# Optimization experiments

Measured on AMD Instinct MI355X. Metric: run time of the kernel, lower is better.

## Reference

```python
import jax, jax.numpy as jnp
import numpy as np

N_EMBD = 1024
N_HEAD = 16
HEAD_DIM = N_EMBD // N_HEAD


def setup_inputs() -> dict:
    key = jax.random.key(0)
    ks = jax.random.split(key, 5)
    B, T = 4, 2048
    s = 0.02
    return {
        "x": jax.random.normal(ks[0], (B, T, N_EMBD), dtype=jnp.float32),
        "w_qkv": jax.random.normal(ks[1], (N_EMBD, 3 * N_EMBD), dtype=jnp.float32) * s,
        "b_qkv": jnp.zeros((3 * N_EMBD,), dtype=jnp.float32),
        "w_out": jax.random.normal(ks[2], (N_EMBD, N_EMBD), dtype=jnp.float32) * s,
        "b_out": jnp.zeros((N_EMBD,), dtype=jnp.float32),
    }


def reference(x, w_qkv, b_qkv, w_out, b_out):
    # Eval-mode forward (dropout disabled), matching the torch module's math.
    B, T, C = x.shape
    qkv = x @ w_qkv + b_qkv                      # [B,T,3C]
    q, k, v = jnp.split(qkv, 3, axis=-1)
    def heads(t):
        return t.reshape(B, T, N_HEAD, HEAD_DIM).transpose(0, 2, 1, 3)  # [B,H,T,D]
    q, k, v = heads(q), heads(k), heads(v)
    scores = jnp.einsum("bhtd,bhsd->bhts", q, k) / jnp.sqrt(jnp.float32(HEAD_DIM))
    causal = jnp.tril(jnp.ones((T, T), dtype=bool))
    scores = jnp.where(causal[None, None], scores, -jnp.inf)
    attn = jax.nn.softmax(scores, axis=-1)       # [B,H,T,T]
    y = jnp.einsum("bhts,bhsd->bhtd", attn, v)   # [B,H,T,D]
    y = y.transpose(0, 2, 1, 3).reshape(B, T, C)
    return y @ w_out + b_out
```

## Files before the change

kernel.cpp:

```cpp
#include <hip/hip_runtime.h>
#include <hip/hip_bf16.h>

#define TSEQ 2048
#define CEMB 1024

typedef __attribute__((ext_vector_type(8))) short bf16x8;
typedef __attribute__((ext_vector_type(4))) float f32x4;
typedef __attribute__((ext_vector_type(16))) float f32x16;
typedef __attribute__((ext_vector_type(4))) int i32x4;

__device__ __forceinline__ unsigned short f2bf(float f){
  return __builtin_bit_cast(unsigned short, __float2bfloat16(f));
}

__device__ __forceinline__ f32x4 MFMA16(bf16x8 a, bf16x8 b, f32x4 c){
  return __builtin_amdgcn_mfma_f32_16x16x32_bf16(a, b, c, 0, 0, 0);
}

#define GLDS(src, dst) __builtin_amdgcn_global_load_lds( \
      (const __attribute__((address_space(1))) void*)(src), \
      (__attribute__((address_space(3))) void*)(dst), 16, 0, 0)

template<int N> __device__ __forceinline__ void vmwait(){
  if constexpr (N == 0) asm volatile("s_waitcnt vmcnt(0)" ::: "memory");
  else if constexpr (N == 6) asm volatile("s_waitcnt vmcnt(6)" ::: "memory");
  else if constexpr (N == 7) asm volatile("s_waitcnt vmcnt(7)" ::: "memory");
  else asm volatile("s_waitcnt vmcnt(8)" ::: "memory");
}

__global__ void k_cvt_bf16(const float* __restrict__ in, unsigned short* __restrict__ out, int n4){
  int i = blockIdx.x * blockDim.x + threadIdx.x;
  if (i >= n4) return;
  const float4 v = reinterpret_cast<const float4*>(in)[i];
  ushort4 o;
  o.x = f2bf(v.x); o.y = f2bf(v.y); o.z = f2bf(v.z); o.w = f2bf(v.w);
  reinterpret_cast<ushort4*>(out)[i] = o;
}

__global__ void k_transpose_bf16(const float* __restrict__ w, unsigned short* __restrict__ wT, int K, int N){
  __shared__ unsigned short tile[32][33];
  const int n0 = blockIdx.x * 32, k0 = blockIdx.y * 32;
  const int tx = threadIdx.x & 31, ty = threadIdx.x >> 5;
  #pragma unroll
  for (int r = 0; r < 4; ++r){
    int k = ty * 4 + r;
    tile[k][tx] = f2bf(w[(size_t)(k0 + k) * N + n0 + tx]);
  }
  __syncthreads();
  #pragma unroll
  for (int r = 0; r < 4; ++r){
    int n = ty * 4 + r;
    wT[(size_t)(n0 + n) * K + k0 + tx] = tile[tx][n];
  }
}

__global__ __launch_bounds__(256) void k_vT(const unsigned short* __restrict__ qkv,
                                            unsigned short* __restrict__ vT){
  __shared__ __align__(16) unsigned short tile[64*64];
  const int tid = threadIdx.x;
  const int bh = blockIdx.x;
  const int t0 = blockIdx.y * 64;
  const int b = bh >> 4, h = bh & 15;
  const int lt = tid >> 3, seg = tid & 7;
  #pragma unroll
  for (int r = 0; r < 2; ++r){
    const int t = lt + 32*r;
    const i32x4 v = *(const i32x4*)&qkv[((size_t)(b*TSEQ + t0 + t))*3072 + 2048 + h*64 + seg*8];
    const int slot = seg ^ (t & 7) ^ (t >> 3);
    *(i32x4*)((char*)tile + t*128 + slot*16) = v;
  }
  __syncthreads();
  const int w = tid >> 6, lane = tid & 63;
  const int tseg = lane & 7;
  #pragma unroll
  for (int r = 0; r < 2; ++r){
    const int d = w*8 + (lane>>3) + 32*r;
    unsigned int wd[4];
    #pragma unroll
    for (int jp = 0; jp < 4; ++jp){
      unsigned int lo, hi;
      #pragma unroll
      for (int e = 0; e < 2; ++e){
        const int j = jp*2 + e;
        const int t = tseg*8 + j;
        const int byteoff = t*128 + ((2*d) ^ (((j ^ tseg) & 7) << 4));
        const unsigned int val = *(const unsigned short*)((const char*)tile + byteoff);
        if (e == 0) lo = val; else hi = val;
      }
      wd[jp] = lo | (hi << 16);
    }
    i32x4 o4; o4[0]=wd[0]; o4[1]=wd[1]; o4[2]=wd[2]; o4[3]=wd[3];
    *(i32x4*)&vT[((size_t)bh*64 + d)*2048 + t0 + tseg*8] = o4;
  }
}

template<bool OUT_BF16, int BN>
__global__ __launch_bounds__(512, 2) void k_gemm256(
    const unsigned short* __restrict__ A,
    const unsigned short* __restrict__ Bt,
    const float* __restrict__ bias,
    void* __restrict__ Cout, int M, int N, int K)
{
  constexpr int NW  = BN / 64;
  constexpr int NH0 = (NW + 1) / 2;
  constexpr int NL  = 4 + NW;
  constexpr int BNB = BN * 128;
  __shared__ __align__(16) char smem[65536 + 2 * BNB];

  const int tid = threadIdx.x;
  const int lane = tid & 63, w = tid >> 6;
  const int wm = w >> 2, wn = w & 3;
  const int l15 = lane & 15, l4 = lane >> 4;
  const int x7 = l15 & 7;

  unsigned lin = blockIdx.x;
  {
    const unsigned nwg = gridDim.x;
    const unsigned qq = nwg >> 3, rr = nwg & 7;
    const unsigned xcd = lin & 7, loc = lin >> 3;
    lin = (xcd < rr ? xcd * (qq + 1) : rr * (qq + 1) + (xcd - rr) * qq) + loc;
  }
  const unsigned ntn = (unsigned)N / BN;
  const int m0 = (int)(lin / ntn) << 8;
  const int n0 = (int)(lin % ntn) * BN;

  const int srow = lane >> 3;
  const int scx  = (lane & 7) ^ srow;
  const unsigned short* Ag = A  + (size_t)(m0 + w*8 + srow) * K + scx * 8;
  const unsigned short* Bg = Bt + (size_t)(n0 + w*8 + srow) * K + scx * 8;

  auto stageA = [&](int buf, int kt){
    const unsigned short* s = Ag + kt*64;
    char* d = smem + buf*32768 + (w << 10);
    #pragma unroll
    for (int i = 0; i < 4; ++i) GLDS(s + (size_t)(i*64)*K, d + i*8192);
  };
  auto stageB = [&](int buf, int kt){
    const unsigned short* s = Bg + kt*64;
    char* d = smem + 65536 + buf*BNB + (w << 10);
    #pragma unroll
    for (int i = 0; i < NW; ++i) GLDS(s + (size_t)(i*64)*K, d + i*8192);
  };

  const int arow = wm*128 + l15;
  const int brow = wn*(BN/4) + l15;
  auto rdA = [&](int buf, int m, int ks)->bf16x8 {
    return *(const bf16x8*)(smem + buf*32768 + (arow + m*16)*128 + (((ks*4 + l4) ^ x7) << 4));
  };
  auto rdB = [&](int buf, int n, int ks)->bf16x8 {
    return *(const bf16x8*)(smem + 65536 + buf*BNB + (brow + n*16)*128 + (((ks*4 + l4) ^ x7) << 4));
  };

  f32x4 acc[8][NW] = {};
  const int NIT = K >> 7;

  stageA(0, 0); stageB(0, 0);
  stageA(1, 1); stageB(1, 1);
  vmwait<NL>();
  __builtin_amdgcn_s_barrier();
  asm volatile("" ::: "memory");

  for (int it = 0; it < NIT; ++it){
    const bool more = (it + 1 < NIT);
    #pragma unroll
    for (int half = 0; half < 2; ++half){
      const int buf = half;
      bf16x8 bfr[NW][2], af1[4][2], af2[4][2];
      #pragma unroll
      for (int n = 0; n < NW; ++n){ bfr[n][0] = rdB(buf, n, 0); bfr[n][1] = rdB(buf, n, 1); }
      #pragma unroll
      for (int m = 0; m < 4; ++m){ af1[m][0] = rdA(buf, m, 0); af1[m][1] = rdA(buf, m, 1); }
      __builtin_amdgcn_s_setprio(1);
      #pragma unroll
      for (int m = 0; m < 4; ++m)
        #pragma unroll
        for (int n = 0; n < NH0; ++n)
          #pragma unroll
          for (int ks = 0; ks < 2; ++ks)
            acc[m][n] = MFMA16(af1[m][ks], bfr[n][ks], acc[m][n]);
      __builtin_amdgcn_s_setprio(0);
      #pragma unroll
      for (int m = 0; m < 4; ++m){ af2[m][0] = rdA(buf, m+4, 0); af2[m][1] = rdA(buf, m+4, 1); }
      __builtin_amdgcn_s_setprio(1);
      #pragma unroll
      for (int m = 0; m < 4; ++m)
        #pragma unroll
        for (int n = NH0; n < NW; ++n)
          #pragma unroll
          for (int ks = 0; ks < 2; ++ks)
            acc[m][n] = MFMA16(af1[m][ks], bfr[n][ks], acc[m][n]);
      __builtin_amdgcn_s_setprio(0);
      __builtin_amdgcn_s_setprio(1);
      #pragma unroll
      for (int m = 0; m < 4; ++m)
        #pragma unroll
        for (int n = NH0; n < NW; ++n)
          #pragma unroll
          for (int ks = 0; ks < 2; ++ks)
            acc[m+4][n] = MFMA16(af2[m][ks], bfr[n][ks], acc[m+4][n]);
      __builtin_amdgcn_s_setprio(0);
      asm volatile("s_waitcnt lgkmcnt(0)" ::: "memory");
      __builtin_amdgcn_s_barrier();
      asm volatile("" ::: "memory");
      if (more){ stageA(buf, 2*it + half + 2); stageB(buf, 2*it + half + 2); }
      __builtin_amdgcn_s_setprio(1);
      #pragma unroll
      for (int m = 0; m < 4; ++m)
        #pragma unroll
        for (int n = 0; n < NH0; ++n)
          #pragma unroll
          for (int ks = 0; ks < 2; ++ks)
            acc[m+4][n] = MFMA16(af2[m][ks], bfr[n][ks], acc[m+4][n]);
      __builtin_amdgcn_s_setprio(0);
      if (more) vmwait<NL>();
      else      vmwait<0>();
      __builtin_amdgcn_s_barrier();
      asm volatile("" ::: "memory");
    }
  }

  float bv[NW];
  #pragma unroll
  for (int n = 0; n < NW; ++n) bv[n] = bias[n0 + wn*(BN/4) + n*16 + l15];

  #pragma unroll
  for (int m = 0; m < 8; ++m){
    const int row = m0 + wm*128 + m*16 + l4*4;
    #pragma unroll
    for (int n = 0; n < NW; ++n){
      const int col = n0 + wn*(BN/4) + n*16 + l15;
      #pragma unroll
      for (int r = 0; r < 4; ++r){
        float v = acc[m][n][r] + bv[n];
        if (OUT_BF16)
          ((unsigned short*)Cout)[(size_t)(row + r) * N + col] = f2bf(v);
        else
          ((float*)Cout)[(size_t)(row + r) * N + col] = v;
      }
    }
  }
}

__global__ __launch_bounds__(512, 4) void k_attn(
    const unsigned short* __restrict__ qkv,
    const unsigned short* __restrict__ vT,
    unsigned short* __restrict__ y)
{
  __shared__ __align__(16) char Ksm[2][8192];
  __shared__ __align__(16) char Vsm[2][8192];
  __shared__ float Ls[8][32];

  const int tid = threadIdx.x, lane = tid & 63, w = tid >> 6;
  const int q31 = lane & 31, hi = lane >> 5;
  const int bh = blockIdx.x, p = blockIdx.y;
  const int g = w >> 2, wl = w & 3;
  const int myt = g ? (15 - p) : p;
  const int b = bh >> 4, h = bh & 15;
  const size_t rowB = (size_t)b * TSEQ;

  const int wq0 = myt*128 + 32*wl, qg = wq0 + q31;
  const int nkt_my = 2*myt + 2;
  const int nktB  = 2*(15 - p) + 2;

  const float sc = 0.18033688011112042f;

  bf16x8 qf[4];
  {
    const unsigned short* qp = qkv + (rowB + qg) * 3072 + h * 64;
    #pragma unroll
    for (int c4 = 0; c4 < 4; ++c4){
      bf16x8 v = *(const bf16x8*)(qp + c4*16 + hi*8);
      #pragma unroll
      for (int j = 0; j < 8; ++j){
        const unsigned int bits = ((unsigned int)(unsigned short)v[j]) << 16;
        v[j] = (short)f2bf(__builtin_bit_cast(float, bits) * sc);
      }
      qf[c4] = v;
    }
  }

  const int kr = lane >> 3, sl = lane & 7, cx = sl ^ kr;
  const unsigned short* kgbase = qkv + (rowB + w*8 + kr) * 3072 + 1024 + h*64 + cx*8;
  const unsigned short* vgbase = vT + ((size_t)bh*64 + w*8 + kr) * 2048 + cx*8;

  #define STAGE(ktile, buf)                                                          \
    do {                                                                             \
      GLDS(kgbase + (size_t)(ktile)*64*3072, &Ksm[buf][0] + w*1024);                 \
      GLDS(vgbase + (ktile)*64,              &Vsm[buf][0] + w*1024);                 \
    } while (0)

  f32x16 O[2] = {};
  float l = 0.f;

  STAGE(0, 0);
  __syncthreads();

  int cbuf = 0;
  for (int kt = 0; kt < nktB; ++kt){
    if (kt + 1 < nktB) STAGE(kt + 1, cbuf ^ 1);

    if (kt < nkt_my){
      const char* kb = Ksm[cbuf];
      const char* vb = Vsm[cbuf];
      const bool domask = (kt*64 + 63 > wq0);
      #pragma unroll
      for (int sub = 0; sub < 2; ++sub){
        f32x16 S = {};
        __builtin_amdgcn_s_setprio(1);
        #pragma unroll
        for (int c4 = 0; c4 < 4; ++c4){
          const bf16x8 kf = *(const bf16x8*)(kb + (sub*32 + q31)*128
                                + ((((c4<<1)|hi) ^ (q31 & 7)) << 4));
          S = __builtin_amdgcn_mfma_f32_32x32x16_bf16(kf, qf[c4], S, 0, 0, 0);
        }
        __builtin_amdgcn_s_setprio(0);
        if (domask){
          #pragma unroll
          for (int r = 0; r < 16; ++r){
            const int kg = kt*64 + sub*32 + (r&3) + 8*(r>>2) + 4*hi;
            if (kg > qg) S[r] = -1e30f;
          }
        }
        float ps = 0.f;
        #pragma unroll
        for (int r = 0; r < 16; ++r){
          S[r] = __builtin_amdgcn_exp2f(S[r]);
          ps += S[r];
        }
        l += ps;
        bf16x8 paf[2];
        #pragma unroll
        for (int kc = 0; kc < 2; ++kc){
          const int e = kc * 8;
          unsigned int a, bb, cc, dd;
          asm("v_cvt_pk_bf16_f32 %0, %1, %2" : "=v"(a)  : "v"(S[e+0]), "v"(S[e+1]));
          asm("v_cvt_pk_bf16_f32 %0, %1, %2" : "=v"(bb) : "v"(S[e+4]), "v"(S[e+5]));
          asm("v_cvt_pk_bf16_f32 %0, %1, %2" : "=v"(cc) : "v"(S[e+2]), "v"(S[e+3]));
          asm("v_cvt_pk_bf16_f32 %0, %1, %2" : "=v"(dd) : "v"(S[e+6]), "v"(S[e+7]));
          asm volatile("v_permlane32_swap_b32 %0, %1" : "+v"(a),  "+v"(bb));
          asm volatile("v_permlane32_swap_b32 %0, %1" : "+v"(cc), "+v"(dd));
          i32x4 pwv; pwv[0] = (int)a; pwv[1] = (int)cc; pwv[2] = (int)bb; pwv[3] = (int)dd;
          paf[kc] = __builtin_bit_cast(bf16x8, pwv);
        }
        __builtin_amdgcn_s_setprio(1);
        #pragma unroll
        for (int kc = 0; kc < 2; ++kc){
          #pragma unroll
          for (int dblk = 0; dblk < 2; ++dblk){
            const int dr = dblk*32 + q31;
            const bf16x8 vf = *(const bf16x8*)(vb + dr*128
                                  + ((((sub<<2)|(kc<<1)|hi) ^ (dr & 7)) << 4));
            O[dblk] = __builtin_amdgcn_mfma_f32_32x32x16_bf16(paf[kc], vf, O[dblk], 0, 0, 0);
          }
        }
        __builtin_amdgcn_s_setprio(0);
      }
    }

    __syncthreads();
    cbuf ^= 1;
  }

  {
    const float lc = l + __shfl_xor(l, 32);
    if (lane < 32) Ls[w][lane] = 1.0f / lc;
  }
  __syncthreads();

  #pragma unroll
  for (int r = 0; r < 16; ++r){
    const int qloc = (r&3) + 8*(r>>2) + 4*hi;
    const float inv = Ls[w][qloc];
    const size_t row = rowB + wq0 + qloc;
    #pragma unroll
    for (int dblk = 0; dblk < 2; ++dblk)
      y[row * CEMB + h*64 + dblk*32 + q31] = f2bf(O[dblk][r] * inv);
  }
  #undef STAGE
}

extern "C" void kernel_launch(void* const* d_in, const int* in_sizes, int n_in,
                              void* d_out, int out_size, void* d_ws, size_t ws_size,
                              hipStream_t stream)
{
  const float* x     = (const float*)d_in[0];
  const float* w_qkv = (const float*)d_in[1];
  const float* b_qkv = (const float*)d_in[2];
  const float* w_out = (const float*)d_in[3];
  const float* b_out = (const float*)d_in[4];
  float* out = (float*)d_out;

  char* ws = (char*)d_ws;
  unsigned short* xb    = (unsigned short*)(ws);
  unsigned short* vTb   = (unsigned short*)(ws);
  unsigned short* qkvb  = (unsigned short*)(ws + (16u<<20));
  unsigned short* yb    = (unsigned short*)(ws + (64u<<20));
  unsigned short* wqkvT = (unsigned short*)(ws + (80u<<20));
  unsigned short* woutT = (unsigned short*)(ws + (86u<<20));

  const int M = 4 * TSEQ;

  k_cvt_bf16<<<(M * CEMB / 4 + 255) / 256, 256, 0, stream>>>(x, xb, M * CEMB / 4);
  k_transpose_bf16<<<dim3(3072/32, 1024/32), 256, 0, stream>>>(w_qkv, wqkvT, 1024, 3072);
  k_transpose_bf16<<<dim3(1024/32, 1024/32), 256, 0, stream>>>(w_out, woutT, 1024, 1024);

  k_gemm256<true, 192><<<dim3((M/256) * (3072/192)), 512, 0, stream>>>(xb, wqkvT, b_qkv, qkvb, M, 3072, 1024);
  k_vT<<<dim3(64, TSEQ/64), 256, 0, stream>>>(qkvb, vTb);
  k_attn<<<dim3(4 * 16, 8), 512, 0, stream>>>(qkvb, vTb, yb);
  k_gemm256<false, 128><<<dim3((M/256) * (1024/128)), 512, 0, stream>>>(yb, woutT, b_out, out, M, 1024, 1024);
}
```

Measured before the change: 159.2 us.

## Balance causal attention work across warp groups and merge prep kernels

The attention kernel now gives both warp groups the same 17 KV tiles. Group A processes its short query tile, writes it out, then helps with part of the long tile B. Group B's partial output and row sums are combined with group A's through shared memory before the final write. This removes the idle time group A had while waiting for group B's longer causal range, at the cost of 64KB of LDS, a separate KV staging buffer per group, and an extra merge step. The bf16 conversion of x and the two weight transposes are also fused into one launch to cut launch overhead.

After: 174.3 us. 9.5% more time.

```diff
diff --git a/kernel.cpp b/kernel.cpp
--- a/kernel.cpp
+++ b/kernel.cpp
@@ -28,19 +28,32 @@
   else asm volatile("s_waitcnt vmcnt(8)" ::: "memory");
 }
 
-__global__ void k_cvt_bf16(const float* __restrict__ in, unsigned short* __restrict__ out, int n4){
-  int i = blockIdx.x * blockDim.x + threadIdx.x;
-  if (i >= n4) return;
-  const float4 v = reinterpret_cast<const float4*>(in)[i];
-  ushort4 o;
-  o.x = f2bf(v.x); o.y = f2bf(v.y); o.z = f2bf(v.z); o.w = f2bf(v.w);
-  reinterpret_cast<ushort4*>(out)[i] = o;
-}
-
-__global__ void k_transpose_bf16(const float* __restrict__ w, unsigned short* __restrict__ wT, int K, int N){
+__global__ __launch_bounds__(256) void k_prep(
+    const float* __restrict__ x, unsigned short* __restrict__ xb,
+    const float* __restrict__ w_qkv, unsigned short* __restrict__ wqkvT,
+    const float* __restrict__ w_out, unsigned short* __restrict__ woutT)
+{
   __shared__ unsigned short tile[32][33];
-  const int n0 = blockIdx.x * 32, k0 = blockIdx.y * 32;
-  const int tx = threadIdx.x & 31, ty = threadIdx.x >> 5;
+  const int bid = blockIdx.x, tid = threadIdx.x;
+  if (bid < 8192){
+    const int i = bid * 256 + tid;
+    const float4 v = reinterpret_cast<const float4*>(x)[i];
+    ushort4 o;
+    o.x = f2bf(v.x); o.y = f2bf(v.y); o.z = f2bf(v.z); o.w = f2bf(v.w);
+    reinterpret_cast<ushort4*>(xb)[i] = o;
+    return;
+  }
+  const float* w; unsigned short* wT; int N, n0, k0;
+  if (bid < 11264){
+    const int b2 = bid - 8192;
+    w = w_qkv; wT = wqkvT; N = 3072;
+    n0 = (b2 % 96) * 32; k0 = (b2 / 96) * 32;
+  } else {
+    const int b3 = bid - 11264;
+    w = w_out; wT = woutT; N = 1024;
+    n0 = (b3 & 31) * 32; k0 = (b3 >> 5) * 32;
+  }
+  const int tx = tid & 31, ty = tid >> 5;
   #pragma unroll
   for (int r = 0; r < 4; ++r){
     int k = ty * 4 + r;
@@ -50,7 +63,7 @@
   #pragma unroll
   for (int r = 0; r < 4; ++r){
     int n = ty * 4 + r;
-    wT[(size_t)(n0 + n) * K + k0 + tx] = tile[tx][n];
+    wT[(size_t)(n0 + n) * 1024 + k0 + tx] = tile[tx][n];
   }
 }
 
@@ -246,27 +259,26 @@
     const unsigned short* __restrict__ vT,
     unsigned short* __restrict__ y)
 {
-  __shared__ __align__(16) char Ksm[2][8192];
-  __shared__ __align__(16) char Vsm[2][8192];
+  __shared__ __align__(16) char smem[65536];
   __shared__ float Ls[8][32];
+  __shared__ float lB[4][32];
 
   const int tid = threadIdx.x, lane = tid & 63, w = tid >> 6;
   const int q31 = lane & 31, hi = lane >> 5;
   const int bh = blockIdx.x, p = blockIdx.y;
   const int g = w >> 2, wl = w & 3;
-  const int myt = g ? (15 - p) : p;
+  const int tA = p, tB = 15 - p;
   const int b = bh >> 4, h = bh & 15;
   const size_t rowB = (size_t)b * TSEQ;
-
-  const int wq0 = myt*128 + 32*wl, qg = wq0 + q31;
-  const int nkt_my = 2*myt + 2;
-  const int nktB  = 2*(15 - p) + 2;
+  const int nktA = 2*p + 2;
 
   const float sc = 0.18033688011112042f;
 
+  int wq0 = (g ? tB : tA) * 128 + 32 * wl;
+
   bf16x8 qf[4];
-  {
-    const unsigned short* qp = qkv + (rowB + qg) * 3072 + h * 64;
+  auto loadQ = [&](int qgx){
+    const unsigned short* qp = qkv + (rowB + qgx) * 3072 + h * 64;
     #pragma unroll
     for (int c4 = 0; c4 < 4; ++c4){
       bf16x8 v = *(const bf16x8*)(qp + c4*16 + hi*8);
@@ -277,106 +289,148 @@
       }
       qf[c4] = v;
     }
-  }
-
-  const int kr = lane >> 3, sl = lane & 7, cx = sl ^ kr;
-  const unsigned short* kgbase = qkv + (rowB + w*8 + kr) * 3072 + 1024 + h*64 + cx*8;
-  const unsigned short* vgbase = vT + ((size_t)bh*64 + w*8 + kr) * 2048 + cx*8;
-
-  #define STAGE(ktile, buf)                                                          \
-    do {                                                                             \
-      GLDS(kgbase + (size_t)(ktile)*64*3072, &Ksm[buf][0] + w*1024);                 \
-      GLDS(vgbase + (ktile)*64,              &Vsm[buf][0] + w*1024);                 \
-    } while (0)
+  };
+  loadQ(wq0 + q31);
+
+  const int kr = lane >> 3, cx = (lane & 7) ^ kr;
+  const unsigned short* kgbase = qkv + (rowB + wl*8 + kr) * 3072 + 1024 + h*64 + cx*8;
+  const unsigned short* vgbase = vT + ((size_t)bh*64 + wl*8 + kr) * 2048 + cx*8;
+  char* const gKV = smem + g*32768;
+
+  auto stage = [&](int kv, int buf){
+    char* kb = gKV + buf*16384;
+    #pragma unroll
+    for (int j = 0; j < 2; ++j){
+      GLDS(kgbase + (size_t)kv*64*3072 + (size_t)j*32*3072, kb + j*4096 + wl*1024);
+      GLDS(vgbase + (size_t)kv*64      + (size_t)j*32*2048, kb + 8192 + j*4096 + wl*1024);
+    }
+  };
+  auto kv_of = [&](int i)->int {
+    return g ? (i + 15 - 2*p) : (i < nktA ? i : i - nktA);
+  };
 
   f32x16 O[2] = {};
   float l = 0.f;
 
-  STAGE(0, 0);
+  auto storeY = [&](int wq0s){
+    const float lc = l + __shfl_xor(l, 32);
+    if (lane < 32) Ls[w][lane] = 1.0f / lc;
+    asm volatile("s_waitcnt lgkmcnt(0)" ::: "memory");
+    #pragma unroll
+    for (int r = 0; r < 16; ++r){
+      const int qloc = (r&3) + 8*(r>>2) + 4*hi;
+      const float inv = Ls[w][qloc];
+      const size_t row = rowB + wq0s + qloc;
+      #pragma unroll
+      for (int dblk = 0; dblk < 2; ++dblk)
+        y[row * CEMB + h*64 + dblk*32 + q31] = f2bf(O[dblk][r] * inv);
+    }
+  };
+
+  stage(kv_of(0), 0);
   __syncthreads();
 
   int cbuf = 0;
-  for (int kt = 0; kt < nktB; ++kt){
-    if (kt + 1 < nktB) STAGE(kt + 1, cbuf ^ 1);
-
-    if (kt < nkt_my){
-      const char* kb = Ksm[cbuf];
-      const char* vb = Vsm[cbuf];
-      const bool domask = (kt*64 + 63 > wq0);
-      #pragma unroll
-      for (int sub = 0; sub < 2; ++sub){
-        f32x16 S = {};
-        __builtin_amdgcn_s_setprio(1);
-        #pragma unroll
-        for (int c4 = 0; c4 < 4; ++c4){
-          const bf16x8 kf = *(const bf16x8*)(kb + (sub*32 + q31)*128
-                                + ((((c4<<1)|hi) ^ (q31 & 7)) << 4));
-          S = __builtin_amdgcn_mfma_f32_32x32x16_bf16(kf, qf[c4], S, 0, 0, 0);
+  for (int i = 0; i < 17; ++i){
+    if (i + 1 < 17) stage(kv_of(i + 1), cbuf ^ 1);
+
+    if (!g && i == nktA){
+      storeY(tA*128 + 32*wl);
+      #pragma unroll
+      for (int dblk = 0; dblk < 2; ++dblk) O[dblk] = (f32x16){};
+      l = 0.f;
+      wq0 = tB*128 + 32*wl;
+      loadQ(wq0 + q31);
+    }
+
+    const int kv = kv_of(i);
+    const int qg = wq0 + q31;
+    const char* kb = gKV + cbuf*16384;
+    const char* vb = kb + 8192;
+    const bool domask = (kv*64 + 63 > wq0);
+    #pragma unroll
+    for (int sub = 0; sub < 2; ++sub){
+      f32x16 S = {};
+      __builtin_amdgcn_s_setprio(1);
+      #pragma unroll
+      for (int c4 = 0; c4 < 4; ++c4){
+        const bf16x8 kf = *(const bf16x8*)(kb + (sub*32 + q31)*128
+                              + ((((c4<<1)|hi) ^ (q31 & 7)) << 4));
+        S = __builtin_amdgcn_mfma_f32_32x32x16_bf16(kf, qf[c4], S, 0, 0, 0);
+      }
+      __builtin_amdgcn_s_setprio(0);
+      if (domask){
+        #pragma unroll
+        for (int r = 0; r < 16; ++r){
+          const int kg = kv*64 + sub*32 + (r&3) + 8*(r>>2) + 4*hi;
+          if (kg > qg) S[r] = -1e30f;
         }
-        __builtin_amdgcn_s_setprio(0);
-        if (domask){
-          #pragma unroll
-          for (int r = 0; r < 16; ++r){
-            const int kg = kt*64 + sub*32 + (r&3) + 8*(r>>2) + 4*hi;
-            if (kg > qg) S[r] = -1e30f;
-          }
+      }
+      float ps = 0.f;
+      #pragma unroll
+      for (int r = 0; r < 16; ++r){
+        S[r] = __builtin_amdgcn_exp2f(S[r]);
+        ps += S[r];
+      }
+      l += ps;
+      bf16x8 paf[2];
+      #pragma unroll
+      for (int kc = 0; kc < 2; ++kc){
+        const int e = kc * 8;
+        unsigned int a, bb, cc, dd;
+        asm("v_cvt_pk_bf16_f32 %0, %1, %2" : "=v"(a)  : "v"(S[e+0]), "v"(S[e+1]));
+        asm("v_cvt_pk_bf16_f32 %0, %1, %2" : "=v"(bb) : "v"(S[e+4]), "v"(S[e+5]));
+        asm("v_cvt_pk_bf16_f32 %0, %1, %2" : "=v"(cc) : "v"(S[e+2]), "v"(S[e+3]));
+        asm("v_cvt_pk_bf16_f32 %0, %1, %2" : "=v"(dd) : "v"(S[e+6]), "v"(S[e+7]));
+        asm volatile("v_permlane32_swap_b32 %0, %1" : "+v"(a),  "+v"(bb));
+        asm volatile("v_permlane32_swap_b32 %0, %1" : "+v"(cc), "+v"(dd));
+        i32x4 pwv; pwv[0] = (int)a; pwv[1] = (int)cc; pwv[2] = (int)bb; pwv[3] = (int)dd;
+        paf[kc] = __builtin_bit_cast(bf16x8, pwv);
+      }
+      __builtin_amdgcn_s_setprio(1);
+      #pragma unroll
+      for (int kc = 0; kc < 2; ++kc){
+        #pragma unroll
+        for (int dblk = 0; dblk < 2; ++dblk){
+          const int dr = dblk*32 + q31;
+          const bf16x8 vf = *(const bf16x8*)(vb + dr*128
+                                + ((((sub<<2)|(kc<<1)|hi) ^ (dr & 7)) << 4));
+          O[dblk] = __builtin_amdgcn_mfma_f32_32x32x16_bf16(paf[kc], vf, O[dblk], 0, 0, 0);
         }
-        float ps = 0.f;
-        #pragma unroll
-        for (int r = 0; r < 16; ++r){
-          S[r] = __builtin_amdgcn_exp2f(S[r]);
-          ps += S[r];
-        }
-        l += ps;
-        bf16x8 paf[2];
-        #pragma unroll
-        for (int kc = 0; kc < 2; ++kc){
-          const int e = kc * 8;
-          unsigned int a, bb, cc, dd;
-          asm("v_cvt_pk_bf16_f32 %0, %1, %2" : "=v"(a)  : "v"(S[e+0]), "v"(S[e+1]));
-          asm("v_cvt_pk_bf16_f32 %0, %1, %2" : "=v"(bb) : "v"(S[e+4]), "v"(S[e+5]));
-          asm("v_cvt_pk_bf16_f32 %0, %1, %2" : "=v"(cc) : "v"(S[e+2]), "v"(S[e+3]));
-          asm("v_cvt_pk_bf16_f32 %0, %1, %2" : "=v"(dd) : "v"(S[e+6]), "v"(S[e+7]));
-          asm volatile("v_permlane32_swap_b32 %0, %1" : "+v"(a),  "+v"(bb));
-          asm volatile("v_permlane32_swap_b32 %0, %1" : "+v"(cc), "+v"(dd));
-          i32x4 pwv; pwv[0] = (int)a; pwv[1] = (int)cc; pwv[2] = (int)bb; pwv[3] = (int)dd;
-          paf[kc] = __builtin_bit_cast(bf16x8, pwv);
-        }
-        __builtin_amdgcn_s_setprio(1);
-        #pragma unroll
-        for (int kc = 0; kc < 2; ++kc){
-          #pragma unroll
-          for (int dblk = 0; dblk < 2; ++dblk){
-            const int dr = dblk*32 + q31;
-            const bf16x8 vf = *(const bf16x8*)(vb + dr*128
-                                  + ((((sub<<2)|(kc<<1)|hi) ^ (dr & 7)) << 4));
-            O[dblk] = __builtin_amdgcn_mfma_f32_32x32x16_bf16(paf[kc], vf, O[dblk], 0, 0, 0);
-          }
-        }
-        __builtin_amdgcn_s_setprio(0);
-      }
+      }
+      __builtin_amdgcn_s_setprio(0);
     }
 
     __syncthreads();
     cbuf ^= 1;
   }
 
-  {
+  float* cb = (float*)smem;
+  if (!g){
+    float* dst = cb + (size_t)(wl*64 + lane) * 33;
+    #pragma unroll
+    for (int dblk = 0; dblk < 2; ++dblk)
+      #pragma unroll
+      for (int r = 0; r < 16; ++r) dst[dblk*16 + r] = O[dblk][r];
     const float lc = l + __shfl_xor(l, 32);
+    if (lane < 32) lB[wl][lane] = lc;
+  }
+  __syncthreads();
+  if (g){
+    const float* src = cb + (size_t)(wl*64 + lane) * 33;
+    const float lc = l + __shfl_xor(l, 32) + lB[wl][q31];
     if (lane < 32) Ls[w][lane] = 1.0f / lc;
-  }
-  __syncthreads();
-
-  #pragma unroll
-  for (int r = 0; r < 16; ++r){
-    const int qloc = (r&3) + 8*(r>>2) + 4*hi;
-    const float inv = Ls[w][qloc];
-    const size_t row = rowB + wq0 + qloc;
-    #pragma unroll
-    for (int dblk = 0; dblk < 2; ++dblk)
-      y[row * CEMB + h*64 + dblk*32 + q31] = f2bf(O[dblk][r] * inv);
-  }
-  #undef STAGE
+    asm volatile("s_waitcnt lgkmcnt(0)" ::: "memory");
+    #pragma unroll
+    for (int r = 0; r < 16; ++r){
+      const int qloc = (r&3) + 8*(r>>2) + 4*hi;
+      const float inv = Ls[w][qloc];
+      const size_t row = rowB + tB*128 + 32*wl + qloc;
+      #pragma unroll
+      for (int dblk = 0; dblk < 2; ++dblk)
+        y[row * CEMB + h*64 + dblk*32 + q31] = f2bf((O[dblk][r] + src[dblk*16 + r]) * inv);
+    }
+  }
 }
 
 extern "C" void kernel_launch(void* const* d_in, const int* in_sizes, int n_in,
@@ -400,9 +454,7 @@
 
   const int M = 4 * TSEQ;
 
-  k_cvt_bf16<<<(M * CEMB / 4 + 255) / 256, 256, 0, stream>>>(x, xb, M * CEMB / 4);
-  k_transpose_bf16<<<dim3(3072/32, 1024/32), 256, 0, stream>>>(w_qkv, wqkvT, 1024, 3072);
-  k_transpose_bf16<<<dim3(1024/32, 1024/32), 256, 0, stream>>>(w_out, woutT, 1024, 1024);
+  k_prep<<<12288, 256, 0, stream>>>(x, xb, w_qkv, wqkvT, w_out, woutT);
 
   k_gemm256<true, 192><<<dim3((M/256) * (3072/192)), 512, 0, stream>>>(xb, wqkvT, b_qkv, qkvb, M, 3072, 1024);
   k_vT<<<dim3(64, TSEQ/64), 256, 0, stream>>>(qkvb, vTb);
```
